# Performance work log

Hardware: AMD Instinct MI355X
Metric: run time of the kernel (lower is better)

The kernel has to match this reference:

```python
import jax, jax.numpy as jnp
import numpy as np

HEADS = 8
DIM = 512
DIM_HEAD = DIM // 8          # 64
LANDMARKS = DIM // 2         # 256
PINV_ITERS = 6
KERNEL = 33                  # residual_conv_kernel default
SCALE = DIM_HEAD ** -0.5


def setup_inputs() -> dict:
    key = jax.random.key(0)
    k0, k1, k2, k3 = jax.random.split(key, 4)
    b, n = 2, 8192
    x = jax.random.normal(k0, (b, n, DIM), dtype=jnp.float32)
    inner = HEADS * DIM_HEAD
    w_qkv = jax.random.normal(k1, (DIM, 3 * inner), dtype=jnp.float32) * 0.02
    w_out = jax.random.normal(k2, (inner, DIM), dtype=jnp.float32) * 0.02
    b_out = jnp.zeros((DIM,), dtype=jnp.float32)
    # grouped depthwise-over-heads conv: (out_ch=H, in_ch/groups=1, kH=33, kW=1)
    w_conv = jax.random.normal(k3, (HEADS, 1, KERNEL, 1), dtype=jnp.float32) * 0.02
    return {"x": x, "w_qkv": w_qkv, "w_out": w_out, "b_out": b_out, "w_conv": w_conv}


def _moore_penrose_pinv(x, iters=PINV_ITERS):
    # x: [b, h, m, m]
    abs_x = jnp.abs(x)
    col = abs_x.sum(axis=-1).max()   # global max over col sums (matches torch.max)
    row = abs_x.sum(axis=-2).max()
    z = jnp.swapaxes(x, -1, -2) / (col * row)
    I = jnp.eye(x.shape[-1], dtype=x.dtype)
    for _ in range(iters):
        xz = x @ z
        z = 0.25 * z @ (13.0 * I - xz @ (15.0 * I - xz @ (7.0 * I - xz)))
    return z


def reference(x, w_qkv, w_out, b_out, w_conv):
    b, n, _ = x.shape
    m = LANDMARKS
    l = n // m  # n chosen divisible by m, so no left-padding branch

    qkv = x @ w_qkv                                   # [b, n, 3*inner]
    q, k, v = jnp.split(qkv, 3, axis=-1)
    to_heads = lambda t: t.reshape(b, n, HEADS, DIM_HEAD).transpose(0, 2, 1, 3)
    q = to_heads(q) * SCALE                           # [b, h, n, d]
    k = to_heads(k)
    v = to_heads(v)

    # landmarks: mean over consecutive groups of l tokens -> [b, h, m, d]
    q_l = q.reshape(b, HEADS, m, l, DIM_HEAD).mean(axis=3)
    k_l = k.reshape(b, HEADS, m, l, DIM_HEAD).mean(axis=3)

    sim1 = jnp.einsum('bhid,bhjd->bhij', q, k_l)      # [b, h, n, m]
    sim2 = jnp.einsum('bhid,bhjd->bhij', q_l, k_l)    # [b, h, m, m]
    sim3 = jnp.einsum('bhid,bhjd->bhij', q_l, k)      # [b, h, m, n]

    attn1 = jax.nn.softmax(sim1, axis=-1)
    attn2 = jax.nn.softmax(sim2, axis=-1)
    attn3 = jax.nn.softmax(sim3, axis=-1)

    attn2_inv = _moore_penrose_pinv(attn2)
    out = attn1 @ (attn2_inv @ (attn3 @ v))           # [b, h, n, d]

    # residual depthwise conv over the sequence dim, per head (groups = heads)
    pad = KERNEL // 2
    res = jax.lax.conv_general_dilated(
        v, w_conv, window_strides=(1, 1), padding=((pad, pad), (0, 0)),
        dimension_numbers=('NCHW', 'OIHW', 'NCHW'), feature_group_count=HEADS)
    out = out + res

    out = out.transpose(0, 2, 1, 3).reshape(b, n, HEADS * DIM_HEAD)
    out = out @ w_out + b_out                         # to_out (dropout = eval no-op)
    return x + out                                    # NyAttenLayer residual
```

## Files before the change

kernel.cpp:

```cpp
#include <hip/hip_runtime.h>
#include <hip/hip_bf16.h>

#define BH 16
#define NTOK 8192
#define NHEAD 8
#define DH 64
#define MLM 256
#define QSCALE 0.125f
#define LP 72

typedef unsigned short ushort_t;
using frag_ab = __attribute__((ext_vector_type(8))) short;
using frag_cd = __attribute__((ext_vector_type(4))) float;

__device__ __forceinline__ unsigned short f2bs(float f){
  __hip_bfloat16 h = __float2bfloat16(f);
  return *(unsigned short*)&h;
}
__device__ __forceinline__ float bs2f(unsigned short u){
  union { unsigned int i; float f; } cv; cv.i = ((unsigned int)u) << 16; return cv.f;
}

__device__ __forceinline__ void gl_lds16(const unsigned short* g, unsigned short* l){
  __builtin_amdgcn_global_load_lds((const __attribute__((address_space(1))) unsigned int*)(const void*)g,
                                   (__attribute__((address_space(3))) unsigned int*)(void*)l, 16, 0, 0);
}

__global__ __launch_bounds__(256) void k_splitw(const float* __restrict__ in, int K, int N,
                                                unsigned short* __restrict__ oh,
                                                unsigned short* __restrict__ ol, int swz){
  const int idx = blockIdx.x * 256 + threadIdx.x;
  const int n = idx / K, k = idx - n * K;
  const float v = in[(size_t)k * N + n];
  const unsigned short hi = f2bs(v);
  int kd = k;
  if (swz){
    const int q = (k >> 3) & 3;
    kd = (k & ~31) | (((q ^ (n & 3)) & 3) << 3) | (k & 7);
  }
  oh[(size_t)n * K + kd] = hi;
  ol[(size_t)n * K + kd] = f2bs(v - bs2f(hi));
}

__global__ __launch_bounds__(256) void k_splitx(const float* __restrict__ in,
                                                unsigned short* __restrict__ oh,
                                                unsigned short* __restrict__ ol){
  const size_t i4 = ((size_t)blockIdx.x * 256 + threadIdx.x) * 4;
  const int row = (int)(i4 >> 9);
  const int col = (int)(i4 & 511);
  const int q = (col >> 3) & 3;
  const int cd = (col & ~31) | (((q ^ (row & 3)) & 3) << 3) | (col & 7);
  const size_t o4 = ((size_t)row << 9) + cd;
  float4 v = *(const float4*)(in + i4);
  const unsigned short h0 = f2bs(v.x), h1 = f2bs(v.y), h2 = f2bs(v.z), h3 = f2bs(v.w);
  *(ushort4*)(oh + o4) = make_ushort4(h0, h1, h2, h3);
  *(ushort4*)(ol + o4) = make_ushort4(f2bs(v.x - bs2f(h0)), f2bs(v.y - bs2f(h1)),
                                      f2bs(v.z - bs2f(h2)), f2bs(v.w - bs2f(h3)));
}

__global__ __launch_bounds__(256) void k_mfma_qkv(const unsigned short* __restrict__ xh,
                                                  const unsigned short* __restrict__ xl,
                                                  const unsigned short* __restrict__ bth,
                                                  const unsigned short* __restrict__ btl,
                                                  float* __restrict__ q,
                                                  unsigned short* __restrict__ kSh,
                                                  unsigned short* __restrict__ kSl,
                                                  float* __restrict__ v){
  const int n0 = blockIdx.x * 128;
  const int m0 = blockIdx.y * 128;
  __shared__ unsigned short Ah[128*32], Al[128*32], Bh[128*32], Bl[128*32];
  const int tid = threadIdx.x;
  const int wave = tid >> 6, lane = tid & 63;
  const int wm = wave >> 1, wn = wave & 1;
  const int lr = lane & 15, quad = lane >> 4;
  const int cswz = ((quad ^ (lr & 3)) & 3) << 3;
  const unsigned short* gsrc = (wave == 0) ? xh : (wave == 1) ? xl : (wave == 2) ? bth : btl;
  unsigned short* lbase = (wave == 0) ? Ah : (wave == 1) ? Al : (wave == 2) ? Bh : Bl;
  const int R0 = (wave < 2) ? m0 : n0;
  const int lrow = lane >> 2, lslot = (lane & 3) << 3;
  frag_cd acc[4][4];
#pragma unroll
  for (int mt = 0; mt < 4; mt++)
#pragma unroll
    for (int nt = 0; nt < 4; nt++){
      frag_cd z = {0.f, 0.f, 0.f, 0.f};
      acc[mt][nt] = z;
    }
  for (int k0 = 0; k0 < 512; k0 += 32){
    __syncthreads();
#pragma unroll
    for (int u = 0; u < 8; u++){
      gl_lds16(gsrc + (size_t)(R0 + u*16 + lrow) * 512 + k0 + lslot, lbase + u * 512);
    }
    __syncthreads();
    frag_ab a_h[4], a_l[4], b_h[4], b_l[4];
#pragma unroll
    for (int t = 0; t < 4; t++){
      const int ar = (wm*64 + t*16 + lr) << 5;
      const int br = (wn*64 + t*16 + lr) << 5;
      a_h[t] = *(const frag_ab*)&Ah[ar + cswz];
      a_l[t] = *(const frag_ab*)&Al[ar + cswz];
      b_h[t] = *(const frag_ab*)&Bh[br + cswz];
      b_l[t] = *(const frag_ab*)&Bl[br + cswz];
    }
#pragma unroll
    for (int mt = 0; mt < 4; mt++)
#pragma unroll
      for (int nt = 0; nt < 4; nt++){
        acc[mt][nt] = __builtin_amdgcn_mfma_f32_16x16x32_bf16(a_l[mt], b_h[nt], acc[mt][nt], 0, 0, 0);
        acc[mt][nt] = __builtin_amdgcn_mfma_f32_16x16x32_bf16(a_h[mt], b_l[nt], acc[mt][nt], 0, 0, 0);
        acc[mt][nt] = __builtin_amdgcn_mfma_f32_16x16x32_bf16(a_h[mt], b_h[nt], acc[mt][nt], 0, 0, 0);
      }
  }
#pragma unroll
  for (int mt = 0; mt < 4; mt++)
#pragma unroll
    for (int nt = 0; nt < 4; nt++)
#pragma unroll
      for (int rg = 0; rg < 4; rg++){
        const int row = m0 + wm*64 + mt*16 + quad*4 + rg;
        const int col = n0 + wn*64 + nt*16 + lr;
        const int bb = row >> 13, i = row & 8191;
        const int which = col >> 9;
        const int cc = col & 511;
        const int h = cc >> 6, d = cc & 63;
        const size_t off = (((size_t)(bb * NHEAD + h)) * NTOK + i) * DH + d;
        const float val = acc[mt][nt][rg];
        if (which == 0)      q[off] = val * QSCALE;
        else if (which == 1){
          const unsigned short hi = f2bs(val);
          kSh[off] = hi; kSl[off] = f2bs(val - bs2f(hi));
        }
        else                 v[off] = val;
      }
}

__global__ __launch_bounds__(256) void k_mfma_final(const unsigned int* __restrict__ qpk,
                                                    const unsigned short* __restrict__ bth,
                                                    const unsigned short* __restrict__ btl,
                                                    const float* __restrict__ xin,
                                                    const float* __restrict__ bout,
                                                    float* __restrict__ outp){
  const int n0 = blockIdx.x * 128;
  const int m0 = blockIdx.y * 128;
  __shared__ unsigned short Ah[128][40], Al[128][40], Bh[128][40], Bl[128][40];
  const int tid = threadIdx.x;
  const int wave = tid >> 6, lane = tid & 63;
  const int wm = wave >> 1, wn = wave & 1;
  const int lr = lane & 15, quad = lane >> 4, koff = quad * 8;
  const int bb = m0 >> 13;
  frag_cd acc[4][4];
#pragma unroll
  for (int mt = 0; mt < 4; mt++)
#pragma unroll
    for (int nt = 0; nt < 4; nt++){
      frag_cd z = {0.f, 0.f, 0.f, 0.f};
      acc[mt][nt] = z;
    }
  for (int k0 = 0; k0 < 512; k0 += 32){
    const int h = k0 >> 6, dbase = k0 & 63;
    __syncthreads();
#pragma unroll
    for (int u = 0; u < 4; u++){
      const int f = tid + u * 256, row = f >> 3, c4 = (f & 7) << 2;
      const int i = (m0 + row) & 8191;
      uint4 pw = *(const uint4*)(qpk + (((size_t)(bb * NHEAD + h)) * NTOK + i) * DH + dbase + c4);
      *(ushort4*)&Ah[row][c4] = make_ushort4((unsigned short)pw.x, (unsigned short)pw.y,
                                             (unsigned short)pw.z, (unsigned short)pw.w);
      *(ushort4*)&Al[row][c4] = make_ushort4((unsigned short)(pw.x >> 16), (unsigned short)(pw.y >> 16),
                                             (unsigned short)(pw.z >> 16), (unsigned short)(pw.w >> 16));
    }
#pragma unroll
    for (int u = 0; u < 2; u++){
      const int f = tid + u * 256, row = f >> 2, ch = (f & 3) << 3;
      *(uint4*)&Bh[row][ch] = *(const uint4*)(bth + (size_t)(n0 + row) * 512 + k0 + ch);
      *(uint4*)&Bl[row][ch] = *(const uint4*)(btl + (size_t)(n0 + row) * 512 + k0 + ch);
    }
    __syncthreads();
    frag_ab a_h[4], a_l[4], b_h[4], b_l[4];
#pragma unroll
    for (int t = 0; t < 4; t++){
      a_h[t] = *(const frag_ab*)&Ah[wm*64 + t*16 + lr][koff];
      a_l[t] = *(const frag_ab*)&Al[wm*64 + t*16 + lr][koff];
      b_h[t] = *(const frag_ab*)&Bh[wn*64 + t*16 + lr][koff];
      b_l[t] = *(const frag_ab*)&Bl[wn*64 + t*16 + lr][koff];
    }
#pragma unroll
    for (int mt = 0; mt < 4; mt++)
#pragma unroll
      for (int nt = 0; nt < 4; nt++){
        acc[mt][nt] = __builtin_amdgcn_mfma_f32_16x16x32_bf16(a_l[mt], b_h[nt], acc[mt][nt], 0, 0, 0);
        acc[mt][nt] = __builtin_amdgcn_mfma_f32_16x16x32_bf16(a_h[mt], b_l[nt], acc[mt][nt], 0, 0, 0);
        acc[mt][nt] = __builtin_amdgcn_mfma_f32_16x16x32_bf16(a_h[mt], b_h[nt], acc[mt][nt], 0, 0, 0);
      }
  }
#pragma unroll
  for (int mt = 0; mt < 4; mt++)
#pragma unroll
    for (int nt = 0; nt < 4; nt++)
#pragma unroll
      for (int rg = 0; rg < 4; rg++){
        const int row = m0 + wm*64 + mt*16 + quad*4 + rg;
        const int col = n0 + wn*64 + nt*16 + lr;
        outp[(size_t)row * 512 + col] = acc[mt][nt][rg] + bout[col] + xin[(size_t)row * 512 + col];
      }
}

__global__ __launch_bounds__(64) void k_land2(const float* __restrict__ qf,
                                              const unsigned short* __restrict__ kSh,
                                              const unsigned short* __restrict__ kSl,
                                              float* __restrict__ qlf, float* __restrict__ klf,
                                              unsigned short* __restrict__ qlSh, unsigned short* __restrict__ qlSl,
                                              unsigned short* __restrict__ klSh, unsigned short* __restrict__ klSl){
  const int isK = blockIdx.y;
  float* dst = isK ? klf : qlf;
  unsigned short* dh = isK ? klSh : qlSh;
  unsigned short* dl = isK ? klSl : qlSl;
  const int bh = blockIdx.x >> 8;
  const int j  = blockIdx.x & 255;
  const int d  = threadIdx.x;
  const size_t base = ((size_t)bh * NTOK + (size_t)j * 32) * DH + d;
  float s = 0.f;
  if (!isK){
    const float* p = qf + base;
#pragma unroll
    for (int t = 0; t < 32; t++) s += p[t * DH];
  } else {
    const unsigned short* ph = kSh + base;
    const unsigned short* pl = kSl + base;
#pragma unroll
    for (int t = 0; t < 32; t++) s += bs2f(ph[t * DH]) + bs2f(pl[t * DH]);
  }
  const float val = s * (1.f / 32.f);
  const size_t oidx = ((size_t)bh * MLM + j) * DH + d;
  dst[oidx] = val;
  const unsigned short hi = f2bs(val);
  dh[oidx] = hi;
  dl[oidx] = f2bs(val - bs2f(hi));
}

__global__ __launch_bounds__(256) void k_vtrans(const float* __restrict__ vf,
                                                unsigned short* __restrict__ vTh,
                                                unsigned short* __restrict__ vTl){
  __shared__ float T[64][68];
  const int j0 = blockIdx.x * 64, bh = blockIdx.y;
  const int tid = threadIdx.x;
#pragma unroll
  for (int u = 0; u < 4; u++){
    const int f = tid + u * 256, row = f >> 4, c4 = (f & 15) << 2;
    *(float4*)&T[row][c4] = *(const float4*)(vf + ((size_t)bh * NTOK + j0 + row) * DH + c4);
  }
  __syncthreads();
#pragma unroll
  for (int u = 0; u < 4; u++){
    const int f = tid + u * 256, d = f >> 4, j4 = (f & 15) << 2;
    const float v0 = T[j4+0][d], v1 = T[j4+1][d], v2 = T[j4+2][d], v3 = T[j4+3][d];
    const unsigned short h0 = f2bs(v0), h1 = f2bs(v1), h2 = f2bs(v2), h3 = f2bs(v3);
    const size_t off = ((size_t)bh * DH + d) * NTOK + j0 + j4;
    *(ushort4*)(vTh + off) = make_ushort4(h0, h1, h2, h3);
    *(ushort4*)(vTl + off) = make_ushort4(f2bs(v0 - bs2f(h0)), f2bs(v1 - bs2f(h1)),
                                          f2bs(v2 - bs2f(h2)), f2bs(v3 - bs2f(h3)));
  }
}

__global__ __launch_bounds__(256) void k_sim2(const float* __restrict__ qlf,
                                              const float* __restrict__ klf,
                                              float* __restrict__ C){
  const int bh = blockIdx.z;
  const float* Ab = qlf + (size_t)bh * MLM * DH;
  const float* Bb = klf + (size_t)bh * MLM * DH;
  float* Cb = C + (size_t)bh * MLM * MLM;
  const int n0 = blockIdx.x * 64;
  const int m0 = blockIdx.y * 64;
  __shared__ float As[16][64];
  __shared__ float Bs[16][64];
  const int tid = threadIdx.x, ty = tid >> 4, tx = tid & 15;
  const int lm = tid >> 2, lk = (tid & 3) << 2;
  float acc[4][4] = {};
  for (int k0 = 0; k0 < 64; k0 += 16){
    float4 a4 = *(const float4*)(Ab + (size_t)(m0 + lm) * DH + k0 + lk);
    As[lk+0][lm] = a4.x; As[lk+1][lm] = a4.y; As[lk+2][lm] = a4.z; As[lk+3][lm] = a4.w;
    float4 b4 = *(const float4*)(Bb + (size_t)(n0 + lm) * DH + k0 + lk);
    Bs[lk+0][lm] = b4.x; Bs[lk+1][lm] = b4.y; Bs[lk+2][lm] = b4.z; Bs[lk+3][lm] = b4.w;
    __syncthreads();
#pragma unroll
    for (int kk = 0; kk < 16; kk++){
      float a[4], bv[4];
#pragma unroll
      for (int r = 0; r < 4; r++) a[r] = As[kk][ty*4 + r];
#pragma unroll
      for (int c = 0; c < 4; c++) bv[c] = Bs[kk][tx*4 + c];
#pragma unroll
      for (int r = 0; r < 4; r++)
#pragma unroll
        for (int c = 0; c < 4; c++) acc[r][c] += a[r] * bv[c];
    }
    __syncthreads();
  }
#pragma unroll
  for (int r = 0; r < 4; r++)
#pragma unroll
    for (int c = 0; c < 4; c++)
      Cb[(size_t)(m0 + ty*4 + r) * MLM + n0 + tx*4 + c] = acc[r][c];
}

__global__ __launch_bounds__(256) void k_softmax256(const float* __restrict__ in, float* __restrict__ outp){
  const int row = blockIdx.x;
  const int t = threadIdx.x;
  float v = in[(size_t)row * 256 + t];
  __shared__ float red[256];
  red[t] = v; __syncthreads();
  for (int o = 128; o > 0; o >>= 1){ if (t < o) red[t] = fmaxf(red[t], red[t+o]); __syncthreads(); }
  float mx = red[0]; __syncthreads();
  float e = expf(v - mx);
  red[t] = e; __syncthreads();
  for (int o = 128; o > 0; o >>= 1){ if (t < o) red[t] += red[t+o]; __syncthreads(); }
  outp[(size_t)row * 256 + t] = e / red[0];
}

__global__ __launch_bounds__(256) void k_colrow(const float* __restrict__ a2, float* __restrict__ part){
  const int bh = blockIdx.x;
  const int t = threadIdx.x;
  const float* p = a2 + (size_t)bh * 65536;
  float cs = 0.f;
  for (int i = 0; i < 256; i++) cs += fabsf(p[(size_t)i * 256 + t]);
  __shared__ float r2[256];
  r2[t] = cs; __syncthreads();
  for (int o = 128; o > 0; o >>= 1){
    if (t < o) r2[t] = fmaxf(r2[t], r2[t+o]);
    __syncthreads();
  }
  if (t == 0) part[bh] = r2[0];
}

__global__ __launch_bounds__(256) void k_z0(const float* __restrict__ a2, const float* __restrict__ part,
                                            float* __restrict__ z,
                                            unsigned short* __restrict__ zTh,
                                            unsigned short* __restrict__ zTl){
  const int bh = blockIdx.x >> 8;
  const int i  = blockIdx.x & 255;
  const int j  = threadIdx.x;
  float m2 = 0.f;
#pragma unroll
  for (int t = 0; t < 16; t++) m2 = fmaxf(m2, part[t]);
  const float sc = 1.f / m2;
  const size_t ridx = ((size_t)bh * 256 + j) * 256 + i;
  const float val = a2[ridx] * sc;
  z[((size_t)bh * 256 + i) * 256 + j] = val;
  const unsigned short hi = f2bs(val);
  zTh[ridx] = hi;
  zTl[ridx] = f2bs(val - bs2f(hi));
}

__global__ __launch_bounds__(256) void k_gemm256m(const float* __restrict__ A,
                                                  const unsigned short* __restrict__ BTh,
                                                  const unsigned short* __restrict__ BTl,
                                                  const float* __restrict__ D,
                                                  float* __restrict__ C,
                                                  unsigned short* __restrict__ CTh,
                                                  unsigned short* __restrict__ CTl,
                                                  float c0, float s0, int wC){
  __shared__ unsigned short Ah[32][40], Al[32][40], Bh[64][40], Bl[64][40];
  __shared__ float Ct[64][33];
  const int bh = blockIdx.y, tile = blockIdx.x;
  const int m0 = (tile >> 2) * 32, n0 = (tile & 3) * 64;
  const size_t bo = (size_t)bh * 65536;
  const int tid = threadIdx.x;
  const int wave = tid >> 6, lane = tid & 63;
  const int wm = wave >> 1, wn = wave & 1;
  const int lr = lane & 15, quad = lane >> 4, koff = quad * 8;
  const int ar = tid >> 3, ac = (tid & 7) << 2;
  const int br = tid >> 2, bc = (tid & 3) << 3;
  frag_cd acc[2];
  { frag_cd z = {0.f,0.f,0.f,0.f}; acc[0] = z; acc[1] = z; }
  float4 ra  = *(const float4*)(A + bo + (size_t)(m0 + ar) * 256 + ac);
  uint4  rbh = *(const uint4*)(BTh + bo + (size_t)(n0 + br) * 256 + bc);
  uint4  rbl = *(const uint4*)(BTl + bo + (size_t)(n0 + br) * 256 + bc);
  for (int k0 = 0; k0 < 256; k0 += 32){
    __syncthreads();
    {
      const unsigned short h0=f2bs(ra.x),h1=f2bs(ra.y),h2=f2bs(ra.z),h3=f2bs(ra.w);
      *(ushort4*)&Ah[ar][ac] = make_ushort4(h0,h1,h2,h3);
      *(ushort4*)&Al[ar][ac] = make_ushort4(f2bs(ra.x-bs2f(h0)), f2bs(ra.y-bs2f(h1)),
                                            f2bs(ra.z-bs2f(h2)), f2bs(ra.w-bs2f(h3)));
      *(uint4*)&Bh[br][bc] = rbh;
      *(uint4*)&Bl[br][bc] = rbl;
    }
    __syncthreads();
    if (k0 < 224){
      ra  = *(const float4*)(A + bo + (size_t)(m0 + ar) * 256 + k0 + 32 + ac);
      rbh = *(const uint4*)(BTh + bo + (size_t)(n0 + br) * 256 + k0 + 32 + bc);
      rbl = *(const uint4*)(BTl + bo + (size_t)(n0 + br) * 256 + k0 + 32 + bc);
    }
    frag_ab a_h = *(const frag_ab*)&Ah[wm*16 + lr][koff];
    frag_ab a_l = *(const frag_ab*)&Al[wm*16 + lr][koff];
#pragma unroll
    for (int b = 0; b < 2; b++){
      frag_ab b_h = *(const frag_ab*)&Bh[wn*32 + b*16 + lr][koff];
      frag_ab b_l = *(const frag_ab*)&Bl[wn*32 + b*16 + lr][koff];
      acc[b] = __builtin_amdgcn_mfma_f32_16x16x32_bf16(a_l, b_l, acc[b], 0, 0, 0);
      acc[b] = __builtin_amdgcn_mfma_f32_16x16x32_bf16(a_l, b_h, acc[b], 0, 0, 0);
      acc[b] = __builtin_amdgcn_mfma_f32_16x16x32_bf16(a_h, b_l, acc[b], 0, 0, 0);
      acc[b] = __builtin_amdgcn_mfma_f32_16x16x32_bf16(a_h, b_h, acc[b], 0, 0, 0);
    }
  }
  const bool useD = (c0 != 0.f);
#pragma unroll
  for (int b = 0; b < 2; b++)
#pragma unroll
    for (int rg = 0; rg < 4; rg++){
      const int row = m0 + wm*16 + quad*4 + rg;
      const int col = n0 + wn*32 + b*16 + lr;
      const size_t idx = bo + (size_t)row * 256 + col;
      const float dv = useD ? D[idx] : 0.f;
      const float val = s0 * (c0 * dv - acc[b][rg]);
      if (wC) C[idx] = val;
      Ct[col - n0][row - m0] = val;
    }
  __syncthreads();
  {
    const int cr = tid >> 2, sg = (tid & 3) << 3;
    unsigned int ph[4], pl[4];
#pragma unroll
    for (int j = 0; j < 4; j++){
      const float v0 = Ct[cr][sg + 2*j], v1 = Ct[cr][sg + 2*j + 1];
      const unsigned short h0 = f2bs(v0), h1 = f2bs(v1);
      ph[j] = (unsigned int)h0 | ((unsigned int)h1 << 16);
      pl[j] = (unsigned int)f2bs(v0 - bs2f(h0)) | ((unsigned int)f2bs(v1 - bs2f(h1)) << 16);
    }
    const size_t tb = bo + (size_t)(n0 + cr) * 256 + m0 + sg;
    *(uint4*)(CTh + tb) = make_uint4(ph[0], ph[1], ph[2], ph[3]);
    *(uint4*)(CTl + tb) = make_uint4(pl[0], pl[1], pl[2], pl[3]);
  }
}

__global__ __launch_bounds__(256) void k_flash(const unsigned short* __restrict__ qlSh,
                                               const unsigned short* __restrict__ qlSl,
                                               const unsigned short* __restrict__ kSh,
                                               const unsigned short* __restrict__ kSl,
                                               const unsigned short* __restrict__ vTh,
                                               const unsigned short* __restrict__ vTl,
                                               float* __restrict__ pbuf){
  extern __shared__ __align__(16) unsigned short sm[];
  unsigned short* Qh  = sm;
  unsigned short* Ql  = sm + 1*64*LP;
  unsigned short* Kh  = sm + 2*64*LP;
  unsigned short* Kl  = sm + 3*64*LP;
  unsigned short* Wth = sm + 4*64*LP;
  unsigned short* Wtl = sm + 5*64*LP;
  unsigned short* Ph  = sm + 6*64*LP;
  unsigned short* Pl  = sm + 7*64*LP;
  const int kc = blockIdx.x, mt = blockIdx.y, bh = blockIdx.z;
  const int m0 = mt * 64, kbeg = kc * 1024;
  const int tid = threadIdx.x;
  const int wave = tid >> 6, lane = tid & 63;
  const int lr = lane & 15, quad = lane >> 4;
  const size_t qbase = (size_t)bh * MLM * DH;
  const size_t kb  = (size_t)bh * NTOK * DH;
  const size_t vtb = (size_t)bh * DH * NTOK;
#pragma unroll
  for (int u = 0; u < 4; u++){
    const int f = tid + u * 256, row = f >> 4, c4 = (f & 15) << 2;
    *(ushort4*)&Qh[row*LP + c4] = *(const ushort4*)(qlSh + qbase + (size_t)(m0 + row) * DH + c4);
    *(ushort4*)&Ql[row*LP + c4] = *(const ushort4*)(qlSl + qbase + (size_t)(m0 + row) * DH + c4);
  }
  float m_run[4], l_run[4];
  frag_cd o[4];
#pragma unroll
  for (int r = 0; r < 4; r++){ m_run[r] = -1e30f; l_run[r] = 0.f; }
#pragma unroll
  for (int nt = 0; nt < 4; nt++){ frag_cd z = {0.f,0.f,0.f,0.f}; o[nt] = z; }

  for (int ch = 0; ch < 16; ch++){
    const int kr0 = kbeg + ch * 64;
    __syncthreads();
#pragma unroll
    for (int u = 0; u < 4; u++){
      const int f = tid + u * 256, row = f >> 4, c4 = (f & 15) << 2;
      *(ushort4*)&Kh[row*LP + c4]  = *(const ushort4*)(kSh + kb + (size_t)(kr0 + row) * DH + c4);
      *(ushort4*)&Kl[row*LP + c4]  = *(const ushort4*)(kSl + kb + (size_t)(kr0 + row) * DH + c4);
      *(ushort4*)&Wth[row*LP + c4] = *(const ushort4*)(vTh + vtb + (size_t)row * NTOK + kr0 + c4);
      *(ushort4*)&Wtl[row*LP + c4] = *(const ushort4*)(vTl + vtb + (size_t)row * NTOK + kr0 + c4);
    }
    __syncthreads();
    frag_cd s[4];
#pragma unroll
    for (int nt = 0; nt < 4; nt++){ frag_cd z = {0.f,0.f,0.f,0.f}; s[nt] = z; }
#pragma unroll
    for (int ks = 0; ks < 2; ks++){
      const int ao = (wave*16 + lr)*LP + ks*32 + quad*8;
      frag_ab a_h = *(const frag_ab*)&Qh[ao];
      frag_ab a_l = *(const frag_ab*)&Ql[ao];
#pragma unroll
      for (int nt = 0; nt < 4; nt++){
        const int bo = (nt*16 + lr)*LP + ks*32 + quad*8;
        frag_ab b_h = *(const frag_ab*)&Kh[bo];
        frag_ab b_l = *(const frag_ab*)&Kl[bo];
        s[nt] = __builtin_amdgcn_mfma_f32_16x16x32_bf16(a_l, b_h, s[nt], 0, 0, 0);
        s[nt] = __builtin_amdgcn_mfma_f32_16x16x32_bf16(a_h, b_l, s[nt], 0, 0, 0);
        s[nt] = __builtin_amdgcn_mfma_f32_16x16x32_bf16(a_h, b_h, s[nt], 0, 0, 0);
      }
    }
#pragma unroll
    for (int rg = 0; rg < 4; rg++){
      float mx = fmaxf(fmaxf(s[0][rg], s[1][rg]), fmaxf(s[2][rg], s[3][rg]));
#pragma unroll
      for (int o2 = 8; o2 >= 1; o2 >>= 1) mx = fmaxf(mx, __shfl_xor(mx, o2));
      const float mnew = fmaxf(m_run[rg], mx);
      float e0 = expf(s[0][rg] - mnew), e1 = expf(s[1][rg] - mnew);
      float e2 = expf(s[2][rg] - mnew), e3 = expf(s[3][rg] - mnew);
      float psum = e0 + e1 + e2 + e3;
#pragma unroll
      for (int o2 = 8; o2 >= 1; o2 >>= 1) psum += __shfl_xor(psum, o2);
      const float alpha = expf(m_run[rg] - mnew);
      l_run[rg] = l_run[rg] * alpha + psum;
      m_run[rg] = mnew;
#pragma unroll
      for (int nt = 0; nt < 4; nt++) o[nt][rg] *= alpha;
      const int prow = (wave*16 + quad*4 + rg) * LP;
      float ee[4] = {e0, e1, e2, e3};
#pragma unroll
      for (int nt = 0; nt < 4; nt++){
        const unsigned short hh = f2bs(ee[nt]);
        Ph[prow + nt*16 + lr] = hh;
        Pl[prow + nt*16 + lr] = f2bs(ee[nt] - bs2f(hh));
      }
    }
#pragma unroll
    for (int ks = 0; ks < 2; ks++){
      const int ao = (wave*16 + lr)*LP + ks*32 + quad*8;
      frag_ab p_h = *(const frag_ab*)&Ph[ao];
      frag_ab p_l = *(const frag_ab*)&Pl[ao];
#pragma unroll
      for (int nt = 0; nt < 4; nt++){
        const int bo = (nt*16 + lr)*LP + ks*32 + quad*8;
        frag_ab b_h = *(const frag_ab*)&Wth[bo];
        frag_ab b_l = *(const frag_ab*)&Wtl[bo];
        o[nt] = __builtin_amdgcn_mfma_f32_16x16x32_bf16(p_l, b_h, o[nt], 0, 0, 0);
        o[nt] = __builtin_amdgcn_mfma_f32_16x16x32_bf16(p_h, b_l, o[nt], 0, 0, 0);
        o[nt] = __builtin_amdgcn_mfma_f32_16x16x32_bf16(p_h, b_h, o[nt], 0, 0, 0);
      }
    }
  }
  float* pb = pbuf + (((size_t)bh * 8 + kc) * 256 + m0) * 68;
#pragma unroll
  for (int rg = 0; rg < 4; rg++){
    const int row = wave*16 + quad*4 + rg;
#pragma unroll
    for (int nt = 0; nt < 4; nt++)
      pb[(size_t)row * 68 + nt*16 + lr] = o[nt][rg];
    if (lr == 0){
      pb[(size_t)row * 68 + 64] = m_run[rg];
      pb[(size_t)row * 68 + 65] = l_run[rg];
    }
  }
}

__global__ __launch_bounds__(256) void k_comb(const float* __restrict__ pbuf, float* __restrict__ av){
  const int wv = threadIdx.x >> 6, lane = threadIdx.x & 63;
  const int id = blockIdx.x * 4 + wv;
  const int bh = id >> 8, row = id & 255;
  const float* base = pbuf + ((size_t)bh * 8 * 256 + row) * 68;
  float M = -1e30f;
#pragma unroll
  for (int k = 0; k < 8; k++) M = fmaxf(M, base[(size_t)k * 256 * 68 + 64]);
  float L = 0.f, o = 0.f;
#pragma unroll
  for (int k = 0; k < 8; k++){
    const float* p = base + (size_t)k * 256 * 68;
    float w = expf(p[64] - M);
    L += p[65] * w;
    o += p[lane] * w;
  }
  av[((size_t)bh * MLM + row) * DH + lane] = o / L;
}

__global__ __launch_bounds__(256) void k_w2(const float* __restrict__ Z, const float* __restrict__ AV,
                                            float* __restrict__ W2,
                                            unsigned short* __restrict__ w2Th,
                                            unsigned short* __restrict__ w2Tl){
  const int bh = blockIdx.y, mt = blockIdx.x;
  const float* Zb = Z + (size_t)bh * 65536;
  const float* Vb = AV + (size_t)bh * MLM * DH;
  float* Wb = W2 + (size_t)bh * MLM * DH;
  const int m0 = mt * 64;
  __shared__ float As[16][64];
  __shared__ float Bs[16][64];
  const int tid = threadIdx.x, ty = tid >> 4, tx = tid & 15;
  const int lm = tid >> 2, lk = (tid & 3) << 2;
  const int lk2 = tid >> 4, ln = (tid & 15) << 2;
  float acc[4][4] = {};
  for (int k0 = 0; k0 < 256; k0 += 16){
    float4 a4 = *(const float4*)(Zb + (size_t)(m0 + lm) * 256 + k0 + lk);
    As[lk+0][lm] = a4.x; As[lk+1][lm] = a4.y; As[lk+2][lm] = a4.z; As[lk+3][lm] = a4.w;
    float4 b4 = *(const float4*)(Vb + (size_t)(k0 + lk2) * DH + ln);
    *(float4*)&Bs[lk2][ln] = b4;
    __syncthreads();
#pragma unroll
    for (int kk = 0; kk < 16; kk++){
      float a[4], bv[4];
#pragma unroll
      for (int r = 0; r < 4; r++) a[r] = As[kk][ty*4 + r];
#pragma unroll
      for (int c = 0; c < 4; c++) bv[c] = Bs[kk][tx*4 + c];
#pragma unroll
      for (int r = 0; r < 4; r++)
#pragma unroll
        for (int c = 0; c < 4; c++) acc[r][c] += a[r] * bv[c];
    }
    __syncthreads();
  }
#pragma unroll
  for (int r = 0; r < 4; r++)
#pragma unroll
    for (int c = 0; c < 4; c++){
      const float val = acc[r][c];
      Wb[(size_t)(m0 + ty*4 + r) * DH + tx*4 + c] = val;
      const unsigned short hi = f2bs(val);
      const size_t tidx = ((size_t)bh * DH + tx*4 + c) * MLM + m0 + ty*4 + r;
      w2Th[tidx] = hi;
      w2Tl[tidx] = f2bs(val - bs2f(hi));
    }
}

__global__ __launch_bounds__(256) void k_attn1(float* __restrict__ qoh,
                                               const unsigned short* __restrict__ klSh,
                                               const unsigned short* __restrict__ klSl,
                                               const float* __restrict__ vf,
                                               const unsigned short* __restrict__ w2Th,
                                               const unsigned short* __restrict__ w2Tl,
                                               const float* __restrict__ wconv){
  extern __shared__ __align__(16) unsigned short sm[];
  unsigned short* Qh  = sm;
  unsigned short* Ql  = sm + 1*64*LP;
  unsigned short* Kh  = sm + 2*64*LP;
  unsigned short* Kl  = sm + 3*64*LP;
  unsigned short* Wth = sm + 4*64*LP;
  unsigned short* Wtl = sm + 5*64*LP;
  unsigned short* Ph  = sm + 6*64*LP;
  unsigned short* Pl  = sm + 7*64*LP;
  float (*Vs)[68] = (float (*)[68])(sm + 2*64*LP);
  float (*St)[68] = (float (*)[68])sm;
  __shared__ float wcs[33];
  const int it = blockIdx.x, bh = blockIdx.y, h = bh & 7;
  const int i0 = it * 64;
  float* qb = qoh + (size_t)bh * NTOK * DH;
  const int tid = threadIdx.x;
  const int wave = tid >> 6, lane = tid & 63;
  const int lr = lane & 15, quad = lane >> 4;
  if (tid < 33) wcs[tid] = wconv[h*33 + tid];
#pragma unroll
  for (int u = 0; u < 4; u++){
    const int f = tid + u * 256, row = f >> 4, c4 = (f & 15) << 2;
    float4 a4 = *(const float4*)(qb + (size_t)(i0 + row) * DH + c4);
    const unsigned short h0 = f2bs(a4.x), h1 = f2bs(a4.y), h2 = f2bs(a4.z), h3 = f2bs(a4.w);
    *(ushort4*)&Qh[row*LP + c4] = make_ushort4(h0, h1, h2, h3);
    *(ushort4*)&Ql[row*LP + c4] = make_ushort4(f2bs(a4.x - bs2f(h0)), f2bs(a4.y - bs2f(h1)),
                                               f2bs(a4.z - bs2f(h2)), f2bs(a4.w - bs2f(h3)));
  }
  float m_run[4], l_run[4];
  frag_cd o[4];
#pragma unroll
  for (int r = 0; r < 4; r++){ m_run[r] = -1e30f; l_run[r] = 0.f; }
#pragma unroll
  for (int nt = 0; nt < 4; nt++){ frag_cd z = {0.f,0.f,0.f,0.f}; o[nt] = z; }
  const size_t klbase = (size_t)bh * MLM * DH;
  const size_t wtbase = (size_t)bh * DH * MLM;

  for (int jc = 0; jc < 4; jc++){
    const int j0 = jc * 64;
    __syncthreads();
#pragma unroll
    for (int u = 0; u < 4; u++){
      const int f = tid + u * 256, row = f >> 4, c4 = (f & 15) << 2;
      *(ushort4*)&Kh[row*LP + c4]  = *(const ushort4*)(klSh + klbase + (size_t)(j0 + row) * DH + c4);
      *(ushort4*)&Kl[row*LP + c4]  = *(const ushort4*)(klSl + klbase + (size_t)(j0 + row) * DH + c4);
      *(ushort4*)&Wth[row*LP + c4] = *(const ushort4*)(w2Th + wtbase + (size_t)row * MLM + j0 + c4);
      *(ushort4*)&Wtl[row*LP + c4] = *(const ushort4*)(w2Tl + wtbase + (size_t)row * MLM + j0 + c4);
    }
    __syncthreads();
    frag_cd s[4];
#pragma unroll
    for (int nt = 0; nt < 4; nt++){ frag_cd z = {0.f,0.f,0.f,0.f}; s[nt] = z; }
#pragma unroll
    for (int ks = 0; ks < 2; ks++){
      const int ao = (wave*16 + lr)*LP + ks*32 + quad*8;
      frag_ab a_h = *(const frag_ab*)&Qh[ao];
      frag_ab a_l = *(const frag_ab*)&Ql[ao];
#pragma unroll
      for (int nt = 0; nt < 4; nt++){
        const int bo = (nt*16 + lr)*LP + ks*32 + quad*8;
        frag_ab b_h = *(const frag_ab*)&Kh[bo];
        frag_ab b_l = *(const frag_ab*)&Kl[bo];
        s[nt] = __builtin_amdgcn_mfma_f32_16x16x32_bf16(a_l, b_h, s[nt], 0, 0, 0);
        s[nt] = __builtin_amdgcn_mfma_f32_16x16x32_bf16(a_h, b_l, s[nt], 0, 0, 0);
        s[nt] = __builtin_amdgcn_mfma_f32_16x16x32_bf16(a_h, b_h, s[nt], 0, 0, 0);
      }
    }
#pragma unroll
    for (int rg = 0; rg < 4; rg++){
      float mx = fmaxf(fmaxf(s[0][rg], s[1][rg]), fmaxf(s[2][rg], s[3][rg]));
#pragma unroll
      for (int o2 = 8; o2 >= 1; o2 >>= 1) mx = fmaxf(mx, __shfl_xor(mx, o2));
      const float mnew = fmaxf(m_run[rg], mx);
      float e0 = expf(s[0][rg] - mnew), e1 = expf(s[1][rg] - mnew);
      float e2 = expf(s[2][rg] - mnew), e3 = expf(s[3][rg] - mnew);
      float psum = e0 + e1 + e2 + e3;
#pragma unroll
      for (int o2 = 8; o2 >= 1; o2 >>= 1) psum += __shfl_xor(psum, o2);
      const float alpha = expf(m_run[rg] - mnew);
      l_run[rg] = l_run[rg] * alpha + psum;
      m_run[rg] = mnew;
#pragma unroll
      for (int nt = 0; nt < 4; nt++) o[nt][rg] *= alpha;
      const int prow = (wave*16 + quad*4 + rg) * LP;
      float ee[4] = {e0, e1, e2, e3};
#pragma unroll
      for (int nt = 0; nt < 4; nt++){
        const unsigned short hh = f2bs(ee[nt]);
        Ph[prow + nt*16 + lr] = hh;
        Pl[prow + nt*16 + lr] = f2bs(ee[nt] - bs2f(hh));
      }
    }
#pragma unroll
    for (int ks = 0; ks < 2; ks++){
      const int ao = (wave*16 + lr)*LP + ks*32 + quad*8;
      frag_ab p_h = *(const frag_ab*)&Ph[ao];
      frag_ab p_l = *(const frag_ab*)&Pl[ao];
#pragma unroll
      for (int nt = 0; nt < 4; nt++){
        const int bo = (nt*16 + lr)*LP + ks*32 + quad*8;
        frag_ab b_h = *(const frag_ab*)&Wth[bo];
        frag_ab b_l = *(const frag_ab*)&Wtl[bo];
        o[nt] = __builtin_amdgcn_mfma_f32_16x16x32_bf16(p_l, b_h, o[nt], 0, 0, 0);
        o[nt] = __builtin_amdgcn_mfma_f32_16x16x32_bf16(p_h, b_l, o[nt], 0, 0, 0);
        o[nt] = __builtin_amdgcn_mfma_f32_16x16x32_bf16(p_h, b_h, o[nt], 0, 0, 0);
      }
    }
  }
#pragma unroll
  for (int rg = 0; rg < 4; rg++){
    const float inv = 1.f / l_run[rg];
#pragma unroll
    for (int nt = 0; nt < 4; nt++) o[nt][rg] *= inv;
  }
  __syncthreads();
#pragma unroll
  for (int u = 0; u < 6; u++){
    const int f = tid + u * 256, row = f >> 4, c4 = (f & 15) << 2;
    const int g = i0 - 16 + row;
    float4 vv = make_float4(0.f, 0.f, 0.f, 0.f);
    if (g >= 0 && g < NTOK) vv = *(const float4*)(vf + ((size_t)bh * NTOK + g) * DH + c4);
    *(float4*)&Vs[row][c4] = vv;
  }
  __syncthreads();
  const int rbase = wave*16 + quad*4;
#pragma unroll
  for (int nt = 0; nt < 4; nt++){
    const int col = nt*16 + lr;
#pragma unroll
    for (int s5 = 0; s5 < 36; s5++){
      const float v = Vs[rbase + s5][col];
#pragma unroll
      for (int rg = 0; rg < 4; rg++){
        const int t = s5 - rg;
        if (t >= 0 && t <= 32) o[nt][rg] += wcs[t] * v;
      }
    }
  }
  __syncthreads();
#pragma unroll
  for (int nt = 0; nt < 4; nt++)
#pragma unroll
    for (int rg = 0; rg < 4; rg++){
      const float val = o[nt][rg];
      const unsigned short hi = f2bs(val);
      const unsigned short lo = f2bs(val - bs2f(hi));
      St[rbase + rg][nt*16 + lr] = __uint_as_float((unsigned int)hi | ((unsigned int)lo << 16));
    }
  __syncthreads();
#pragma unroll
  for (int u = 0; u < 4; u++){
    const int f = tid + u * 256, row = f >> 4, c4 = (f & 15) << 2;
    *(float4*)(qb + (size_t)(i0 + row) * DH + c4) = *(const float4*)&St[row][c4];
  }
}

extern "C" void kernel_launch(void* const* d_in, const int* in_sizes, int n_in,
                              void* d_out, int out_size, void* d_ws, size_t ws_size,
                              hipStream_t stream){
  (void)in_sizes; (void)n_in; (void)out_size; (void)ws_size;
  const float* x     = (const float*)d_in[0];
  const float* wqkv  = (const float*)d_in[1];
  const float* wout  = (const float*)d_in[2];
  const float* bout  = (const float*)d_in[3];
  const float* wconv = (const float*)d_in[4];
  float* outp = (float*)d_out;

  char* base = (char*)d_ws;
  auto alloc = [&](size_t bytes)->char*{
    char* p = base; base += (bytes + 255) & ~(size_t)255; return p;
  };
  const size_t QS = (size_t)BH * NTOK * DH;
  const size_t LS = (size_t)BH * MLM * DH;
  const size_t MM = (size_t)BH * MLM * MLM;

  float* qf   = (float*)alloc(QS * 4);
  float* vf   = (float*)alloc(QS * 4);
  unsigned short* kSh = (unsigned short*)alloc(QS * 2);
  unsigned short* kSl = (unsigned short*)alloc(QS * 2);
  float* qlf  = (float*)alloc(LS * 4);
  float* klf  = (float*)alloc(LS * 4);
  float* a2   = (float*)alloc(MM * 4);
  float* zb   = (float*)alloc(MM * 4);
  float* z2   = (float*)alloc(MM * 4);
  float* xz   = (float*)alloc(MM * 4);
  float* t2   = (float*)alloc(MM * 4);
  float* t4   = (float*)alloc(MM * 4);
  float* part = (float*)alloc(64 * 4);
  char* un = alloc(10 * MM * 2);
  unsigned short* pl0 = (unsigned short*)un;
  unsigned short* zbTh = pl0 + 0*MM; unsigned short* zbTl = pl0 + 1*MM;
  unsigned short* z2Th = pl0 + 2*MM; unsigned short* z2Tl = pl0 + 3*MM;
  unsigned short* xzTh = pl0 + 4*MM; unsigned short* xzTl = pl0 + 5*MM;
  unsigned short* t2Th = pl0 + 6*MM; unsigned short* t2Tl = pl0 + 7*MM;
  unsigned short* t4Th = pl0 + 8*MM; unsigned short* t4Tl = pl0 + 9*MM;
  float* pbuf = (float*)un;
  float* av   = (float*)alloc(LS * 4);
  float* w2   = (float*)alloc(LS * 4);
  unsigned short* wqTh = (unsigned short*)alloc((size_t)1536 * 512 * 2);
  unsigned short* wqTl = (unsigned short*)alloc((size_t)1536 * 512 * 2);
  unsigned short* woTh = (unsigned short*)alloc((size_t)512 * 512 * 2);
  unsigned short* woTl = (unsigned short*)alloc((size_t)512 * 512 * 2);
  unsigned short* qlSh = (unsigned short*)alloc(LS * 2);
  unsigned short* qlSl = (unsigned short*)alloc(LS * 2);
  unsigned short* klSh = (unsigned short*)alloc(LS * 2);
  unsigned short* klSl = (unsigned short*)alloc(LS * 2);
  unsigned short* w2Th = (unsigned short*)alloc(LS * 2);
  unsigned short* w2Tl = (unsigned short*)alloc(LS * 2);
  unsigned short* vTh  = (unsigned short*)alloc(QS * 2);
  unsigned short* vTl  = (unsigned short*)alloc(QS * 2);
  unsigned short* xh = vTh;
  unsigned short* xl = vTl;

  k_splitw<<<1536 * 512 / 256, 256, 0, stream>>>(wqkv, 512, 1536, wqTh, wqTl, 1);
  k_splitw<<<512 * 512 / 256, 256, 0, stream>>>(wout, 512, 512, woTh, woTl, 0);
  k_splitx<<<8192, 256, 0, stream>>>(x, xh, xl);
  k_mfma_qkv<<<dim3(12, 128), 256, 0, stream>>>(xh, xl, wqTh, wqTl, qf, kSh, kSl, vf);
  k_vtrans<<<dim3(NTOK / 64, BH), 256, 0, stream>>>(vf, vTh, vTl);
  k_land2<<<dim3(BH * MLM, 2), 64, 0, stream>>>(qf, kSh, kSl, qlf, klf, qlSh, qlSl, klSh, klSl);
  k_sim2<<<dim3(4, 4, BH), 256, 0, stream>>>(qlf, klf, xz);
  k_softmax256<<<BH * MLM, 256, 0, stream>>>(xz, a2);
  k_colrow<<<BH, 256, 0, stream>>>(a2, part);
  k_z0<<<BH * MLM, 256, 0, stream>>>(a2, part, zb, zbTh, zbTl);
  {
    float* zc = zb;  unsigned short* zcTh = zbTh; unsigned short* zcTl = zbTl;
    float* zn = z2;  unsigned short* znTh = z2Th; unsigned short* znTl = z2Tl;
    for (int it = 0; it < 6; ++it){
      k_gemm256m<<<dim3(32, BH), 256, 0, stream>>>(a2, zcTh, zcTl, a2, xz, xzTh, xzTl, 0.f, -1.f, 1);
      k_gemm256m<<<dim3(32, BH), 256, 0, stream>>>(xz, xzTh, xzTl, xz, t2, t2Th, t2Tl, 7.f, 1.f, 0);
      k_gemm256m<<<dim3(32, BH), 256, 0, stream>>>(xz, t2Th, t2Tl, xz, t4, t4Th, t4Tl, 15.f, 1.f, 0);
      k_gemm256m<<<dim3(32, BH), 256, 0, stream>>>(zc, t4Th, t4Tl, zc, zn, znTh, znTl, 13.f, 0.25f, 1);
      float* tf = zc; zc = zn; zn = tf;
      unsigned short* th = zcTh; zcTh = znTh; znTh = th;
      unsigned short* tl = zcTl; zcTl = znTl; znTl = tl;
    }
  }
  const size_t FLASH_LDS = (size_t)8 * 64 * LP * 2;
  k_flash<<<dim3(8, 4, BH), 256, FLASH_LDS, stream>>>(qlSh, qlSl, kSh, kSl, vTh, vTl, pbuf);
  k_comb<<<BH * MLM / 4, 256, 0, stream>>>(pbuf, av);
  k_w2<<<dim3(4, BH), 256, 0, stream>>>(zb, av, w2, w2Th, w2Tl);
  k_attn1<<<dim3(128, BH), 256, FLASH_LDS, stream>>>(qf, klSh, klSl, vf, w2Th, w2Tl, wconv);
  k_mfma_final<<<dim3(4, 128), 256, 0, stream>>>((const unsigned int*)qf, woTh, woTl, x, bout, outp);
}
```

Measured before the change: 741.4 us.

## Halve flash-attention LDS footprint via register-held Q and buffer aliasing, double split-K

In both k_flash and k_attn1, the Q fragments are loaded once into registers rather than re-read from LDS every chunk. The Q and P tiles are aliased onto the K buffers, guarded by an extra barrier, which halves dynamic shared memory per block so more blocks can be resident per CU. k_flash also splits the key range into 16 chunks of 512 instead of 8 of 1024, giving twice as many blocks, and k_comb now merges 16 partials. The costs are an added __syncthreads per chunk, more register pressure, and twice the partial-buffer traffic. The code relies on pbuf being large enough for 16 partials and on Vs and St being safe to alias at the same offset in k_attn1.

```diff
diff --git a/kernel.cpp b/kernel.cpp
--- a/kernel.cpp
+++ b/kernel.cpp
@@ -442,16 +442,12 @@
                                                const unsigned short* __restrict__ vTl,
                                                float* __restrict__ pbuf){
   extern __shared__ __align__(16) unsigned short sm[];
-  unsigned short* Qh  = sm;
-  unsigned short* Ql  = sm + 1*64*LP;
-  unsigned short* Kh  = sm + 2*64*LP;
-  unsigned short* Kl  = sm + 3*64*LP;
-  unsigned short* Wth = sm + 4*64*LP;
-  unsigned short* Wtl = sm + 5*64*LP;
-  unsigned short* Ph  = sm + 6*64*LP;
-  unsigned short* Pl  = sm + 7*64*LP;
+  unsigned short* Kh  = sm;
+  unsigned short* Kl  = sm + 1*64*LP;
+  unsigned short* Wth = sm + 2*64*LP;
+  unsigned short* Wtl = sm + 3*64*LP;
   const int kc = blockIdx.x, mt = blockIdx.y, bh = blockIdx.z;
-  const int m0 = mt * 64, kbeg = kc * 1024;
+  const int m0 = mt * 64, kbeg = kc * 512;
   const int tid = threadIdx.x;
   const int wave = tid >> 6, lane = tid & 63;
   const int lr = lane & 15, quad = lane >> 4;
@@ -461,8 +457,16 @@
 #pragma unroll
   for (int u = 0; u < 4; u++){
     const int f = tid + u * 256, row = f >> 4, c4 = (f & 15) << 2;
-    *(ushort4*)&Qh[row*LP + c4] = *(const ushort4*)(qlSh + qbase + (size_t)(m0 + row) * DH + c4);
-    *(ushort4*)&Ql[row*LP + c4] = *(const ushort4*)(qlSl + qbase + (size_t)(m0 + row) * DH + c4);
+    *(ushort4*)&Kh[row*LP + c4] = *(const ushort4*)(qlSh + qbase + (size_t)(m0 + row) * DH + c4);
+    *(ushort4*)&Kl[row*LP + c4] = *(const ushort4*)(qlSl + qbase + (size_t)(m0 + row) * DH + c4);
+  }
+  __syncthreads();
+  frag_ab qa_h[2], qa_l[2];
+#pragma unroll
+  for (int ks = 0; ks < 2; ks++){
+    const int ao = (wave*16 + lr)*LP + ks*32 + quad*8;
+    qa_h[ks] = *(const frag_ab*)&Kh[ao];
+    qa_l[ks] = *(const frag_ab*)&Kl[ao];
   }
   float m_run[4], l_run[4];
   frag_cd o[4];
@@ -471,7 +475,7 @@
 #pragma unroll
   for (int nt = 0; nt < 4; nt++){ frag_cd z = {0.f,0.f,0.f,0.f}; o[nt] = z; }
 
-  for (int ch = 0; ch < 16; ch++){
+  for (int ch = 0; ch < 8; ch++){
     const int kr0 = kbeg + ch * 64;
     __syncthreads();
 #pragma unroll
@@ -488,19 +492,17 @@
     for (int nt = 0; nt < 4; nt++){ frag_cd z = {0.f,0.f,0.f,0.f}; s[nt] = z; }
 #pragma unroll
     for (int ks = 0; ks < 2; ks++){
-      const int ao = (wave*16 + lr)*LP + ks*32 + quad*8;
-      frag_ab a_h = *(const frag_ab*)&Qh[ao];
-      frag_ab a_l = *(const frag_ab*)&Ql[ao];
 #pragma unroll
       for (int nt = 0; nt < 4; nt++){
         const int bo = (nt*16 + lr)*LP + ks*32 + quad*8;
         frag_ab b_h = *(const frag_ab*)&Kh[bo];
         frag_ab b_l = *(const frag_ab*)&Kl[bo];
-        s[nt] = __builtin_amdgcn_mfma_f32_16x16x32_bf16(a_l, b_h, s[nt], 0, 0, 0);
-        s[nt] = __builtin_amdgcn_mfma_f32_16x16x32_bf16(a_h, b_l, s[nt], 0, 0, 0);
-        s[nt] = __builtin_amdgcn_mfma_f32_16x16x32_bf16(a_h, b_h, s[nt], 0, 0, 0);
-      }
-    }
+        s[nt] = __builtin_amdgcn_mfma_f32_16x16x32_bf16(qa_l[ks], b_h, s[nt], 0, 0, 0);
+        s[nt] = __builtin_amdgcn_mfma_f32_16x16x32_bf16(qa_h[ks], b_l, s[nt], 0, 0, 0);
+        s[nt] = __builtin_amdgcn_mfma_f32_16x16x32_bf16(qa_h[ks], b_h, s[nt], 0, 0, 0);
+      }
+    }
+    __syncthreads();
 #pragma unroll
     for (int rg = 0; rg < 4; rg++){
       float mx = fmaxf(fmaxf(s[0][rg], s[1][rg]), fmaxf(s[2][rg], s[3][rg]));
@@ -522,15 +524,15 @@
 #pragma unroll
       for (int nt = 0; nt < 4; nt++){
         const unsigned short hh = f2bs(ee[nt]);
-        Ph[prow + nt*16 + lr] = hh;
-        Pl[prow + nt*16 + lr] = f2bs(ee[nt] - bs2f(hh));
+        Kh[prow + nt*16 + lr] = hh;
+        Kl[prow + nt*16 + lr] = f2bs(ee[nt] - bs2f(hh));
       }
     }
 #pragma unroll
     for (int ks = 0; ks < 2; ks++){
       const int ao = (wave*16 + lr)*LP + ks*32 + quad*8;
-      frag_ab p_h = *(const frag_ab*)&Ph[ao];
-      frag_ab p_l = *(const frag_ab*)&Pl[ao];
+      frag_ab p_h = *(const frag_ab*)&Kh[ao];
+      frag_ab p_l = *(const frag_ab*)&Kl[ao];
 #pragma unroll
       for (int nt = 0; nt < 4; nt++){
         const int bo = (nt*16 + lr)*LP + ks*32 + quad*8;
@@ -542,7 +544,7 @@
       }
     }
   }
-  float* pb = pbuf + (((size_t)bh * 8 + kc) * 256 + m0) * 68;
+  float* pb = pbuf + (((size_t)bh * 16 + kc) * 256 + m0) * 68;
 #pragma unroll
   for (int rg = 0; rg < 4; rg++){
     const int row = wave*16 + quad*4 + rg;
@@ -560,13 +562,13 @@
   const int wv = threadIdx.x >> 6, lane = threadIdx.x & 63;
   const int id = blockIdx.x * 4 + wv;
   const int bh = id >> 8, row = id & 255;
-  const float* base = pbuf + ((size_t)bh * 8 * 256 + row) * 68;
+  const float* base = pbuf + ((size_t)bh * 16 * 256 + row) * 68;
   float M = -1e30f;
 #pragma unroll
-  for (int k = 0; k < 8; k++) M = fmaxf(M, base[(size_t)k * 256 * 68 + 64]);
+  for (int k = 0; k < 16; k++) M = fmaxf(M, base[(size_t)k * 256 * 68 + 64]);
   float L = 0.f, o = 0.f;
 #pragma unroll
-  for (int k = 0; k < 8; k++){
+  for (int k = 0; k < 16; k++){
     const float* p = base + (size_t)k * 256 * 68;
     float w = expf(p[64] - M);
     L += p[65] * w;
@@ -631,15 +633,11 @@
                                                const unsigned short* __restrict__ w2Tl,
                                                const float* __restrict__ wconv){
   extern __shared__ __align__(16) unsigned short sm[];
-  unsigned short* Qh  = sm;
-  unsigned short* Ql  = sm + 1*64*LP;
-  unsigned short* Kh  = sm + 2*64*LP;
-  unsigned short* Kl  = sm + 3*64*LP;
-  unsigned short* Wth = sm + 4*64*LP;
-  unsigned short* Wtl = sm + 5*64*LP;
-  unsigned short* Ph  = sm + 6*64*LP;
-  unsigned short* Pl  = sm + 7*64*LP;
-  float (*Vs)[68] = (float (*)[68])(sm + 2*64*LP);
+  unsigned short* Kh  = sm;
+  unsigned short* Kl  = sm + 1*64*LP;
+  unsigned short* Wth = sm + 2*64*LP;
+  unsigned short* Wtl = sm + 3*64*LP;
+  float (*Vs)[68] = (float (*)[68])sm;
   float (*St)[68] = (float (*)[68])sm;
   __shared__ float wcs[33];
   const int it = blockIdx.x, bh = blockIdx.y, h = bh & 7;
@@ -654,9 +652,17 @@
     const int f = tid + u * 256, row = f >> 4, c4 = (f & 15) << 2;
     float4 a4 = *(const float4*)(qb + (size_t)(i0 + row) * DH + c4);
     const unsigned short h0 = f2bs(a4.x), h1 = f2bs(a4.y), h2 = f2bs(a4.z), h3 = f2bs(a4.w);
-    *(ushort4*)&Qh[row*LP + c4] = make_ushort4(h0, h1, h2, h3);
-    *(ushort4*)&Ql[row*LP + c4] = make_ushort4(f2bs(a4.x - bs2f(h0)), f2bs(a4.y - bs2f(h1)),
+    *(ushort4*)&Kh[row*LP + c4] = make_ushort4(h0, h1, h2, h3);
+    *(ushort4*)&Kl[row*LP + c4] = make_ushort4(f2bs(a4.x - bs2f(h0)), f2bs(a4.y - bs2f(h1)),
                                                f2bs(a4.z - bs2f(h2)), f2bs(a4.w - bs2f(h3)));
+  }
+  __syncthreads();
+  frag_ab qa_h[2], qa_l[2];
+#pragma unroll
+  for (int ks = 0; ks < 2; ks++){
+    const int ao = (wave*16 + lr)*LP + ks*32 + quad*8;
+    qa_h[ks] = *(const frag_ab*)&Kh[ao];
+    qa_l[ks] = *(const frag_ab*)&Kl[ao];
   }
   float m_run[4], l_run[4];
   frag_cd o[4];
@@ -684,19 +690,17 @@
     for (int nt = 0; nt < 4; nt++){ frag_cd z = {0.f,0.f,0.f,0.f}; s[nt] = z; }
 #pragma unroll
     for (int ks = 0; ks < 2; ks++){
-      const int ao = (wave*16 + lr)*LP + ks*32 + quad*8;
-      frag_ab a_h = *(const frag_ab*)&Qh[ao];
-      frag_ab a_l = *(const frag_ab*)&Ql[ao];
 #pragma unroll
       for (int nt = 0; nt < 4; nt++){
         const int bo = (nt*16 + lr)*LP + ks*32 + quad*8;
         frag_ab b_h = *(const frag_ab*)&Kh[bo];
         frag_ab b_l = *(const frag_ab*)&Kl[bo];
-        s[nt] = __builtin_amdgcn_mfma_f32_16x16x32_bf16(a_l, b_h, s[nt], 0, 0, 0);
-        s[nt] = __builtin_amdgcn_mfma_f32_16x16x32_bf16(a_h, b_l, s[nt], 0, 0, 0);
-        s[nt] = __builtin_amdgcn_mfma_f32_16x16x32_bf16(a_h, b_h, s[nt], 0, 0, 0);
-      }
-    }
+        s[nt] = __builtin_amdgcn_mfma_f32_16x16x32_bf16(qa_l[ks], b_h, s[nt], 0, 0, 0);
+        s[nt] = __builtin_amdgcn_mfma_f32_16x16x32_bf16(qa_h[ks], b_l, s[nt], 0, 0, 0);
+        s[nt] = __builtin_amdgcn_mfma_f32_16x16x32_bf16(qa_h[ks], b_h, s[nt], 0, 0, 0);
+      }
+    }
+    __syncthreads();
 #pragma unroll
     for (int rg = 0; rg < 4; rg++){
       float mx = fmaxf(fmaxf(s[0][rg], s[1][rg]), fmaxf(s[2][rg], s[3][rg]));
@@ -718,15 +722,15 @@
 #pragma unroll
       for (int nt = 0; nt < 4; nt++){
         const unsigned short hh = f2bs(ee[nt]);
-        Ph[prow + nt*16 + lr] = hh;
-        Pl[prow + nt*16 + lr] = f2bs(ee[nt] - bs2f(hh));
+        Kh[prow + nt*16 + lr] = hh;
+        Kl[prow + nt*16 + lr] = f2bs(ee[nt] - bs2f(hh));
       }
     }
 #pragma unroll
     for (int ks = 0; ks < 2; ks++){
       const int ao = (wave*16 + lr)*LP + ks*32 + quad*8;
-      frag_ab p_h = *(const frag_ab*)&Ph[ao];
-      frag_ab p_l = *(const frag_ab*)&Pl[ao];
+      frag_ab p_h = *(const frag_ab*)&Kh[ao];
+      frag_ab p_l = *(const frag_ab*)&Kl[ao];
 #pragma unroll
       for (int nt = 0; nt < 4; nt++){
         const int bo = (nt*16 + lr)*LP + ks*32 + quad*8;
@@ -866,8 +870,8 @@
       unsigned short* tl = zcTl; zcTl = znTl; znTl = tl;
     }
   }
-  const size_t FLASH_LDS = (size_t)8 * 64 * LP * 2;
-  k_flash<<<dim3(8, 4, BH), 256, FLASH_LDS, stream>>>(qlSh, qlSl, kSh, kSl, vTh, vTl, pbuf);
+  const size_t FLASH_LDS = (size_t)4 * 64 * LP * 2;
+  k_flash<<<dim3(16, 4, BH), 256, FLASH_LDS, stream>>>(qlSh, qlSl, kSh, kSl, vTh, vTl, pbuf);
   k_comb<<<BH * MLM / 4, 256, 0, stream>>>(pbuf, av);
   k_w2<<<dim3(4, BH), 256, 0, stream>>>(zb, av, w2, w2Th, w2Tl);
   k_attn1<<<dim3(128, BH), 256, FLASH_LDS, stream>>>(qf, klSh, klSl, vf, w2Th, w2Tl, wconv);
```

New measurement: 715.7 us. 3.5% less time.
